# Optimization experiments

Hardware: AMD Instinct MI355X
Metric: run time of the kernel (lower is better)

The kernel has to match this reference:

```python
import jax, jax.numpy as jnp
import numpy as np

S1, S2, S3 = 1024, 1024, 32
R = 16  # r1 = r2 = r3


def setup_inputs() -> dict:
    key = jax.random.key(0)
    ks = jax.random.split(key, 7)
    # TR factors (xavier-normal-ish scale)
    Z1 = jax.random.normal(ks[0], (R, S1, R), dtype=jnp.float32) * 0.05
    Z2 = jax.random.normal(ks[1], (R, S2, R), dtype=jnp.float32) * 0.05
    Z3 = jax.random.normal(ks[2], (R, S3, R), dtype=jnp.float32) * 0.05
    # NoFC_3 conv head params (OIHW)
    W1 = jax.random.normal(ks[3], (S3, S3, 3, 3), dtype=jnp.float32) * 0.05
    b1 = jax.random.normal(ks[4], (S3,), dtype=jnp.float32) * 0.05
    W2 = jax.random.normal(ks[5], (S3, S3, 3, 3), dtype=jnp.float32) * 0.05
    b2 = jax.random.normal(ks[6], (S3,), dtype=jnp.float32) * 0.05
    return {"Z1": Z1, "Z2": Z2, "Z3": Z3, "W1": W1, "b1": b1, "W2": W2, "b2": b2}


def _leaky(x):
    # nn.LeakyReLU default negative_slope = 0.01
    return jnp.where(x >= 0, x, 0.01 * x)


def _conv(x, W, b):
    # 3x3, stride 1, SAME padding, NCHW / OIHW
    y = jax.lax.conv_general_dilated(
        x, W, window_strides=(1, 1), padding="SAME",
        dimension_numbers=("NCHW", "OIHW", "NCHW"))
    return y + b[None, :, None, None]


def reference(Z1, Z2, Z3, W1, b1, W2, b2):
    # tr_product: X[i,j,k] = sum_{a,b,c} Z1[a,i,b] Z2[b,j,c] Z3[c,k,a]
    # Contract small factors first to avoid an O(S1*S2) rank-expanded intermediate.
    T = jnp.einsum("cka,aib->kicb", Z3, Z1)        # (S3, S1, r3, r2) — small
    X = jnp.einsum("kicb,bjc->ijk", T, Z2)         # (S1, S2, S3)
    # NoHiT.forward: permute(2,1,0).unsqueeze(0) -> (1, S3, S2, S1)
    x = X.transpose(2, 1, 0)[None]
    x = _leaky(_conv(x, W1, b1))
    x = _leaky(_conv(x, W2, b2))
    # squeeze(0).permute(1,2,0) -> (S2, S1, S3)
    return x[0].transpose(1, 2, 0)
```

## Files before the change

### kernel.cpp

```cpp
#include <hip/hip_runtime.h>

typedef short  s16x4 __attribute__((ext_vector_type(4)));
typedef short  s16x8 __attribute__((ext_vector_type(8)));
typedef float  f32x4 __attribute__((ext_vector_type(4)));
typedef float  f32x16 __attribute__((ext_vector_type(16)));

__device__ __forceinline__ unsigned short f2b(float f) {
    unsigned u = __float_as_uint(f);
    u = u + 0x7FFFu + ((u >> 16) & 1u);
    return (unsigned short)(u >> 16);
}

__device__ __forceinline__ void gload16(const void* g, void* l) {
    __builtin_amdgcn_global_load_lds((const __attribute__((address_space(1))) unsigned*)g,
                                     (__attribute__((address_space(3))) unsigned*)l,
                                     16, 0, 0);
}

__device__ __forceinline__ int swz(int x) { return (x ^ (x >> 2)) & 3; }
__device__ __forceinline__ int f2s(int o) { return (o >> 1) & 3; }

__global__ __launch_bounds__(256) void v_kernel(const float* __restrict__ Z2,
                                                const float* __restrict__ Z3,
                                                short* __restrict__ Bv2) {
    __shared__ float z3t[8192];
    __shared__ float z2s[256];
    const int tid = threadIdx.x, j = blockIdx.x;
    for (int t = tid; t < 8192; t += 256) {
        float v = Z3[t];
        int c = t >> 9, k = (t >> 4) & 31, a = t & 15;
        z3t[c * 512 + a * 32 + k] = v;
    }
    z2s[tid] = Z2[(tid >> 4) * 16384 + j * 16 + (tid & 15)];
    __syncthreads();
    const int a = tid >> 4, b = tid & 15;
    float z2r[16];
    #pragma unroll
    for (int c = 0; c < 16; ++c) z2r[c] = z2s[b * 16 + c];
    float s[32];
    #pragma unroll
    for (int k = 0; k < 32; ++k) s[k] = 0.f;
    #pragma unroll
    for (int c = 0; c < 16; ++c) {
        #pragma unroll
        for (int k4 = 0; k4 < 8; ++k4) {
            f32x4 v = *(const f32x4*)&z3t[c * 512 + a * 32 + k4 * 4];
            #pragma unroll
            for (int r = 0; r < 4; ++r) s[k4 * 4 + r] += z2r[c] * v[r];
        }
    }
    #pragma unroll
    for (int k = 0; k < 32; ++k)
        Bv2[(size_t)(j * 32 + k) * 256 + tid] = (short)f2b(s[k]);
}

__global__ __launch_bounds__(256) void z1r_kernel(const float* __restrict__ Z1,
                                                  short* __restrict__ Z1r) {
    __shared__ float z1s[4096];
    const int tid = threadIdx.x, i0 = blockIdx.x * 16;
    #pragma unroll
    for (int a = 0; a < 16; ++a)
        z1s[a * 256 + tid] = Z1[a * 16384 + i0 * 16 + tid];
    __syncthreads();
    #pragma unroll
    for (int il = 0; il < 16; ++il)
        Z1r[(size_t)(i0 + il) * 256 + tid] =
            (short)f2b(z1s[(tid >> 4) * 256 + il * 16 + (tid & 15)]);
}

__global__ __launch_bounds__(256) void gemm_kernel(const short* __restrict__ Bv2,
                                                   const short* __restrict__ Z1r,
                                                   short* __restrict__ X) {
    __shared__ short sA[128 * 32];
    __shared__ short sB[128 * 32];
    const int tid = threadIdx.x;
    const int w = tid >> 6, lane = tid & 63, lane15 = lane & 15, q = lane >> 4;
    const int wm = w >> 1, wn = w & 1;
    const int bid = blockIdx.x;
    const int l = (bid & 7) * 256 + (bid >> 3);
    const int n0 = (l >> 3) * 128, i0 = (l & 7) * 128;
    const int rs = lane >> 2, sp = lane & 3;
    const int scol = (sp ^ swz(rs)) << 3;
    const int fl = swz(lane15);

    f32x4 acc[4][4];
    #pragma unroll
    for (int a = 0; a < 4; ++a)
        #pragma unroll
        for (int b = 0; b < 4; ++b) acc[a][b] = (f32x4)0;

    for (int kk = 0; kk < 256; kk += 32) {
        gload16(&Bv2[(size_t)(n0 + w * 16 + rs) * 256 + kk + scol],       (char*)sA + w * 1024);
        gload16(&Bv2[(size_t)(n0 + (w + 4) * 16 + rs) * 256 + kk + scol], (char*)sA + (w + 4) * 1024);
        gload16(&Z1r[(size_t)(i0 + w * 16 + rs) * 256 + kk + scol],       (char*)sB + w * 1024);
        gload16(&Z1r[(size_t)(i0 + (w + 4) * 16 + rs) * 256 + kk + scol], (char*)sB + (w + 4) * 1024);
        __syncthreads();
        s16x8 af[4], bf[4];
        #pragma unroll
        for (int fm = 0; fm < 4; ++fm) {
            const int r = wm * 64 + fm * 16 + lane15;
            af[fm] = *(const s16x8*)&sA[r * 32 + ((q ^ fl) << 3)];
        }
        #pragma unroll
        for (int fn = 0; fn < 4; ++fn) {
            const int r = wn * 64 + fn * 16 + lane15;
            bf[fn] = *(const s16x8*)&sB[r * 32 + ((q ^ fl) << 3)];
        }
        #pragma unroll
        for (int fm = 0; fm < 4; ++fm)
            #pragma unroll
            for (int fn = 0; fn < 4; ++fn)
                acc[fm][fn] = __builtin_amdgcn_mfma_f32_16x16x32_bf16(af[fm], bf[fn], acc[fm][fn], 0, 0, 0);
        __syncthreads();
    }

    #pragma unroll
    for (int fm = 0; fm < 4; ++fm) {
        const int nbase = n0 + wm * 64 + fm * 16;
        const int j = nbase >> 5;
        const int k0 = (nbase & 31) + q * 4;
        #pragma unroll
        for (int fn = 0; fn < 4; ++fn) {
            const int i = i0 + wn * 64 + fn * 16 + lane15;
            s16x4 p;
            #pragma unroll
            for (int r = 0; r < 4; ++r) p[r] = (short)f2b(acc[fm][fn][r]);
            *(s16x4*)&X[(size_t)j * 32768 + i * 32 + k0] = p;
        }
    }
}

#define XWN 130
#define XRN (XWN * 32)
__global__ __launch_bounds__(512) void fconv_kernel(const short* __restrict__ in,
                                                    const float* __restrict__ W1,
                                                    const float* __restrict__ b1,
                                                    const float* __restrict__ W2,
                                                    const float* __restrict__ b2,
                                                    float* __restrict__ out) {
    __shared__ short xr[4 * XRN];
    __shared__ short yr[4 * XRN];
    const int tid = threadIdx.x;
    const int w = tid >> 6, lane = tid & 63, r31 = lane & 31, h = lane >> 5;
    const int bx = blockIdx.x, by = blockIdx.y;
    const int x0 = bx * 126, y0 = by * 16;
    const bool isC1 = (w < 4);
    const int tb = isC1 ? (w * 32 - 1) : ((w - 4) * 32);

    s16x8 aw[9][2];
    {
        const float* Ws = isC1 ? W1 : W2;
        #pragma unroll
        for (int t = 0; t < 9; ++t)
            #pragma unroll
            for (int kh = 0; kh < 2; ++kh) {
                const int c0 = kh * 16 + h * 8;
                s16x8 a;
                #pragma unroll
                for (int e = 0; e < 8; ++e)
                    a[e] = (short)f2b(Ws[(r31 * 32 + c0 + e) * 9 + t]);
                aw[t][kh] = a;
            }
    }
    f32x4 bb[4];
    {
        const float* bs = isC1 ? b1 : b2;
        #pragma unroll
        for (int g = 0; g < 4; ++g) bb[g] = *(const f32x4*)&bs[g * 8 + h * 4];
    }

    if (bx == 0 || bx == 8) {
        s16x8* p = (s16x8*)xr;
        for (int i = tid; i < 4 * XWN * 4; i += 512) p[i] = (s16x8)0;
        __syncthreads();
    }

    auto stage = [&](int rho) {
        const int gy = y0 + rho;
        char* base = (char*)&xr[((rho + 4) & 3) * XRN];
        if ((unsigned)gy < 1024u) {
            {
                const int ox = tid >> 2, u = tid & 3;
                const int gx = x0 - 2 + ox;
                if ((unsigned)gx < 1024u)
                    gload16(&in[(size_t)((gy << 10) + gx) * 32 + ((u ^ f2s(ox)) << 3)],
                            base + (w * 64) * 16);
            }
            {
                const int idx = 512 + tid;
                if (idx < XWN * 4) {
                    const int ox = idx >> 2, u = idx & 3;
                    const int gx = x0 - 2 + ox;
                    if ((unsigned)gx < 1024u)
                        gload16(&in[(size_t)((gy << 10) + gx) * 32 + ((u ^ f2s(ox)) << 3)],
                                base + 512 * 16);
                }
            }
        } else {
            s16x8* b8 = (s16x8*)base;
            for (int i = tid; i < XWN * 4; i += 512) b8[i] = (s16x8)0;
        }
    };

    auto conv1_row = [&](int ry) {
        const int gy1 = y0 + ry;
        const int ysl = ((ry + 4) & 3) * XRN;
        if ((unsigned)gy1 < 1024u) {
            int xs[3];
            #pragma unroll
            for (int dy = 0; dy < 3; ++dy) xs[dy] = ((ry - 1 + dy + 4) & 3) * XRN;
            f32x16 acc = (f32x16)0;
            #pragma unroll
            for (int dy = 0; dy < 3; ++dy)
                #pragma unroll
                for (int dx = 0; dx < 3; ++dx) {
                    const int ox = tb + r31 + dx + 1;
                    const int fo = f2s(ox);
                    #pragma unroll
                    for (int kh = 0; kh < 2; ++kh) {
                        const s16x8 bfr = *(const s16x8*)&xr[xs[dy] + ox * 32 + (((kh * 2 + h) ^ fo) << 3)];
                        acc = __builtin_amdgcn_mfma_f32_32x32x16_bf16(aw[dy * 3 + dx][kh], bfr, acc, 0, 0, 0);
                    }
                }
            const int p = tb + r31;
            const int oy = p + 1;
            const int gx1 = x0 + p;
            const bool valid = (unsigned)gx1 < 1024u;
            const int fo = f2s(oy);
            #pragma unroll
            for (int g = 0; g < 4; ++g) {
                s16x4 pk;
                #pragma unroll
                for (int e = 0; e < 4; ++e) {
                    float f = acc[g * 4 + e] + bb[g][e];
                    f = f >= 0.f ? f : 0.01f * f;
                    pk[e] = valid ? (short)f2b(f) : (short)0;
                }
                *(s16x4*)&yr[ysl + oy * 32 + ((g ^ fo) << 3) + h * 4] = pk;
            }
        } else {
            s16x8* b8 = (s16x8*)&yr[ysl];
            for (int i = tid; i < XWN * 4; i += 256) b8[i] = (s16x8)0;
        }
    };

    auto conv2_row = [&](int ro) {
        const int gy = y0 + ro;
        int ys[3];
        #pragma unroll
        for (int dy = 0; dy < 3; ++dy) ys[dy] = ((ro - 1 + dy + 4) & 3) * XRN;
        f32x16 acc = (f32x16)0;
        #pragma unroll
        for (int dy = 0; dy < 3; ++dy)
            #pragma unroll
            for (int dx = 0; dx < 3; ++dx) {
                const int oy = tb + r31 + dx;
                const int fo = f2s(oy);
                #pragma unroll
                for (int kh = 0; kh < 2; ++kh) {
                    const s16x8 bfr = *(const s16x8*)&yr[ys[dy] + oy * 32 + (((kh * 2 + h) ^ fo) << 3)];
                    acc = __builtin_amdgcn_mfma_f32_32x32x16_bf16(aw[dy * 3 + dx][kh], bfr, acc, 0, 0, 0);
                }
            }
        const int px = tb + r31;
        const int gx = x0 + px;
        if (px < 126 && gx < 1024) {
            #pragma unroll
            for (int g = 0; g < 4; ++g) {
                f32x4 v;
                #pragma unroll
                for (int e = 0; e < 4; ++e) {
                    float f = acc[g * 4 + e] + bb[g][e];
                    v[e] = f >= 0.f ? f : 0.01f * f;
                }
                *(f32x4*)&out[(size_t)((gy << 10) + gx) * 32 + g * 8 + h * 4] = v;
            }
        }
    };

    stage(-2); stage(-1); stage(0);
    __syncthreads();

    for (int t = 0; t <= 18; ++t) {
        if (t <= 16) stage(t + 1);
        if (isC1) { if (t <= 17) conv1_row(t - 1); }
        else      { if (t >= 3)  conv2_row(t - 3); }
        __syncthreads();
    }
}

extern "C" void kernel_launch(void* const* d_in, const int* in_sizes, int n_in,
                              void* d_out, int out_size, void* d_ws, size_t ws_size,
                              hipStream_t stream) {
    const float* Z1 = (const float*)d_in[0];
    const float* Z2 = (const float*)d_in[1];
    const float* Z3 = (const float*)d_in[2];
    const float* W1 = (const float*)d_in[3];
    const float* b1 = (const float*)d_in[4];
    const float* W2 = (const float*)d_in[5];
    const float* b2 = (const float*)d_in[6];

    short* X   = (short*)d_ws;
    short* Bv2 = (short*)d_out;
    short* Z1r = Bv2 + 8388608;

    v_kernel  <<<1024, 256, 0, stream>>>(Z2, Z3, Bv2);
    z1r_kernel<<<64,   256, 0, stream>>>(Z1, Z1r);
    gemm_kernel<<<2048, 256, 0, stream>>>(Bv2, Z1r, X);
    fconv_kernel<<<dim3(9, 64), 512, 0, stream>>>(X, W1, b1, W2, b2, (float*)d_out);
}
```

Measured before the change: 151.4 us.

## Make fused conv per-wave independent with direct global loads and no block barriers

The two-conv kernel is restructured so each wave owns its own 30-column by 16-row strip and does conv1 then conv2 itself. Conv1 now loads its input straight from global memory into registers instead of staging rows through shared memory. Intermediate rows go into a small per-wave LDS ring, so the kernel needs no block-wide __syncthreads and no split between producer and consumer waves. In exchange, each wave computes 32 columns to produce 30, and overlapping input rows and columns are re-read from global memory through the caches.

Result: slower. 240.8 us (+59.0%).

```diff
diff --git a/kernel.cpp b/kernel.cpp
--- a/kernel.cpp
+++ b/kernel.cpp
@@ -130,162 +130,141 @@
     }
 }
 
-#define XWN 130
-#define XRN (XWN * 32)
-__global__ __launch_bounds__(512) void fconv_kernel(const short* __restrict__ in,
+#define YRS (34 * 32)
+__global__ __launch_bounds__(256) void fconv_kernel(const short* __restrict__ in,
                                                     const float* __restrict__ W1,
                                                     const float* __restrict__ b1,
                                                     const float* __restrict__ W2,
                                                     const float* __restrict__ b2,
                                                     float* __restrict__ out) {
-    __shared__ short xr[4 * XRN];
-    __shared__ short yr[4 * XRN];
+    __shared__ short yb[4 * 3 * YRS];
     const int tid = threadIdx.x;
-    const int w = tid >> 6, lane = tid & 63, r31 = lane & 31, h = lane >> 5;
-    const int bx = blockIdx.x, by = blockIdx.y;
-    const int x0 = bx * 126, y0 = by * 16;
-    const bool isC1 = (w < 4);
-    const int tb = isC1 ? (w * 32 - 1) : ((w - 4) * 32);
-
-    s16x8 aw[9][2];
+    const int w = tid >> 6, lane = tid & 63, p = lane & 31, h = lane >> 5;
+    const int job = blockIdx.x * 4 + w;
+    const int st = job % 35, bnd = job / 35;
+    const int sx0 = st * 30, y0 = bnd * 16;
+    short* ybw = &yb[w * 3 * YRS];
+
+    s16x8 aw1[9][2], aw2[9][2];
     {
-        const float* Ws = isC1 ? W1 : W2;
         #pragma unroll
         for (int t = 0; t < 9; ++t)
             #pragma unroll
             for (int kh = 0; kh < 2; ++kh) {
                 const int c0 = kh * 16 + h * 8;
-                s16x8 a;
-                #pragma unroll
-                for (int e = 0; e < 8; ++e)
-                    a[e] = (short)f2b(Ws[(r31 * 32 + c0 + e) * 9 + t]);
-                aw[t][kh] = a;
-            }
-    }
-    f32x4 bb[4];
-    {
-        const float* bs = isC1 ? b1 : b2;
-        #pragma unroll
-        for (int g = 0; g < 4; ++g) bb[g] = *(const f32x4*)&bs[g * 8 + h * 4];
-    }
-
-    if (bx == 0 || bx == 8) {
-        s16x8* p = (s16x8*)xr;
-        for (int i = tid; i < 4 * XWN * 4; i += 512) p[i] = (s16x8)0;
-        __syncthreads();
-    }
-
-    auto stage = [&](int rho) {
-        const int gy = y0 + rho;
-        char* base = (char*)&xr[((rho + 4) & 3) * XRN];
-        if ((unsigned)gy < 1024u) {
-            {
-                const int ox = tid >> 2, u = tid & 3;
-                const int gx = x0 - 2 + ox;
-                if ((unsigned)gx < 1024u)
-                    gload16(&in[(size_t)((gy << 10) + gx) * 32 + ((u ^ f2s(ox)) << 3)],
-                            base + (w * 64) * 16);
-            }
-            {
-                const int idx = 512 + tid;
-                if (idx < XWN * 4) {
-                    const int ox = idx >> 2, u = idx & 3;
-                    const int gx = x0 - 2 + ox;
-                    if ((unsigned)gx < 1024u)
-                        gload16(&in[(size_t)((gy << 10) + gx) * 32 + ((u ^ f2s(ox)) << 3)],
-                                base + 512 * 16);
-                }
-            }
-        } else {
-            s16x8* b8 = (s16x8*)base;
-            for (int i = tid; i < XWN * 4; i += 512) b8[i] = (s16x8)0;
-        }
-    };
-
-    auto conv1_row = [&](int ry) {
-        const int gy1 = y0 + ry;
-        const int ysl = ((ry + 4) & 3) * XRN;
-        if ((unsigned)gy1 < 1024u) {
-            int xs[3];
-            #pragma unroll
-            for (int dy = 0; dy < 3; ++dy) xs[dy] = ((ry - 1 + dy + 4) & 3) * XRN;
+                s16x8 a1, a2;
+                #pragma unroll
+                for (int e = 0; e < 8; ++e) {
+                    a1[e] = (short)f2b(W1[(p * 32 + c0 + e) * 9 + t]);
+                    a2[e] = (short)f2b(W2[(p * 32 + c0 + e) * 9 + t]);
+                }
+                aw1[t][kh] = a1; aw2[t][kh] = a2;
+            }
+    }
+    f32x4 bb1[4], bb2[4];
+    #pragma unroll
+    for (int g = 0; g < 4; ++g) {
+        bb1[g] = *(const f32x4*)&b1[g * 8 + h * 4];
+        bb2[g] = *(const f32x4*)&b2[g * 8 + h * 4];
+    }
+
+    bool pxok[3];
+    #pragma unroll
+    for (int dx = 0; dx < 3; ++dx) pxok[dx] = (unsigned)(sx0 - 2 + p + dx) < 1024u;
+    const bool y1ok = (unsigned)(sx0 - 1 + p) < 1024u;
+    const int gx = sx0 + p;
+    const bool outok = (p < 30) && (gx < 1024);
+    const int fop = f2s(p);
+
+    for (int rr = 0; rr <= 18; ++rr) {
+        const int ry = y0 - 1 + rr;
+
+        s16x8 xf2[6];
+        {
+            const int gy = ry + 1;
+            const bool rok = (rr <= 17) && ((unsigned)gy < 1024u);
+            const short* rbase = in + (((size_t)gy << 10) + (sx0 - 2 + p)) * 32 + h * 8;
+            #pragma unroll
+            for (int dx = 0; dx < 3; ++dx)
+                #pragma unroll
+                for (int kh = 0; kh < 2; ++kh) {
+                    s16x8 v = (s16x8)0;
+                    if (rok && pxok[dx]) v = *(const s16x8*)(rbase + dx * 32 + kh * 16);
+                    xf2[dx * 2 + kh] = v;
+                }
+        }
+
+        if (rr >= 3) {
+            const int ro = y0 + rr - 3;
             f32x16 acc = (f32x16)0;
             #pragma unroll
-            for (int dy = 0; dy < 3; ++dy)
+            for (int dy = 0; dy < 3; ++dy) {
+                const int ysl = ((rr - 3 + dy) % 3) * YRS;
                 #pragma unroll
                 for (int dx = 0; dx < 3; ++dx) {
-                    const int ox = tb + r31 + dx + 1;
-                    const int fo = f2s(ox);
+                    const int idx = p + dx;
+                    const int fo = f2s(idx);
                     #pragma unroll
                     for (int kh = 0; kh < 2; ++kh) {
-                        const s16x8 bfr = *(const s16x8*)&xr[xs[dy] + ox * 32 + (((kh * 2 + h) ^ fo) << 3)];
-                        acc = __builtin_amdgcn_mfma_f32_32x32x16_bf16(aw[dy * 3 + dx][kh], bfr, acc, 0, 0, 0);
+                        const s16x8 bfr = *(const s16x8*)&ybw[ysl + idx * 32 + (((kh * 2 + h) ^ fo) << 3)];
+                        acc = __builtin_amdgcn_mfma_f32_32x32x16_bf16(aw2[dy * 3 + dx][kh], bfr, acc, 0, 0, 0);
                     }
                 }
-            const int p = tb + r31;
-            const int oy = p + 1;
-            const int gx1 = x0 + p;
-            const bool valid = (unsigned)gx1 < 1024u;
-            const int fo = f2s(oy);
-            #pragma unroll
-            for (int g = 0; g < 4; ++g) {
-                s16x4 pk;
-                #pragma unroll
-                for (int e = 0; e < 4; ++e) {
-                    float f = acc[g * 4 + e] + bb[g][e];
-                    f = f >= 0.f ? f : 0.01f * f;
-                    pk[e] = valid ? (short)f2b(f) : (short)0;
-                }
-                *(s16x4*)&yr[ysl + oy * 32 + ((g ^ fo) << 3) + h * 4] = pk;
-            }
-        } else {
-            s16x8* b8 = (s16x8*)&yr[ysl];
-            for (int i = tid; i < XWN * 4; i += 256) b8[i] = (s16x8)0;
-        }
-    };
-
-    auto conv2_row = [&](int ro) {
-        const int gy = y0 + ro;
-        int ys[3];
-        #pragma unroll
-        for (int dy = 0; dy < 3; ++dy) ys[dy] = ((ro - 1 + dy + 4) & 3) * XRN;
-        f32x16 acc = (f32x16)0;
-        #pragma unroll
-        for (int dy = 0; dy < 3; ++dy)
-            #pragma unroll
-            for (int dx = 0; dx < 3; ++dx) {
-                const int oy = tb + r31 + dx;
-                const int fo = f2s(oy);
-                #pragma unroll
-                for (int kh = 0; kh < 2; ++kh) {
-                    const s16x8 bfr = *(const s16x8*)&yr[ys[dy] + oy * 32 + (((kh * 2 + h) ^ fo) << 3)];
-                    acc = __builtin_amdgcn_mfma_f32_32x32x16_bf16(aw[dy * 3 + dx][kh], bfr, acc, 0, 0, 0);
-                }
-            }
-        const int px = tb + r31;
-        const int gx = x0 + px;
-        if (px < 126 && gx < 1024) {
-            #pragma unroll
-            for (int g = 0; g < 4; ++g) {
-                f32x4 v;
-                #pragma unroll
-                for (int e = 0; e < 4; ++e) {
-                    float f = acc[g * 4 + e] + bb[g][e];
-                    v[e] = f >= 0.f ? f : 0.01f * f;
-                }
-                *(f32x4*)&out[(size_t)((gy << 10) + gx) * 32 + g * 8 + h * 4] = v;
-            }
-        }
-    };
-
-    stage(-2); stage(-1); stage(0);
-    __syncthreads();
-
-    for (int t = 0; t <= 18; ++t) {
-        if (t <= 16) stage(t + 1);
-        if (isC1) { if (t <= 17) conv1_row(t - 1); }
-        else      { if (t >= 3)  conv2_row(t - 3); }
-        __syncthreads();
+            }
+            if (outok) {
+                #pragma unroll
+                for (int g = 0; g < 4; ++g) {
+                    f32x4 v;
+                    #pragma unroll
+                    for (int e = 0; e < 4; ++e) {
+                        float f = acc[g * 4 + e] + bb2[g][e];
+                        v[e] = f >= 0.f ? f : 0.01f * f;
+                    }
+                    *(f32x4*)&out[(((size_t)ro << 10) + gx) * 32 + g * 8 + h * 4] = v;
+                }
+            }
+        }
+
+        if (rr <= 17) {
+            const int ysl = (rr % 3) * YRS;
+            if ((unsigned)ry < 1024u) {
+                f32x16 acc = (f32x16)0;
+                #pragma unroll
+                for (int dy = 0; dy < 2; ++dy) {
+                    const int gy = ry - 1 + dy;
+                    const bool rok = (unsigned)gy < 1024u;
+                    const short* rbase = in + (((size_t)gy << 10) + (sx0 - 2 + p)) * 32 + h * 8;
+                    #pragma unroll
+                    for (int dx = 0; dx < 3; ++dx)
+                        #pragma unroll
+                        for (int kh = 0; kh < 2; ++kh) {
+                            s16x8 v = (s16x8)0;
+                            if (rok && pxok[dx]) v = *(const s16x8*)(rbase + dx * 32 + kh * 16);
+                            acc = __builtin_amdgcn_mfma_f32_32x32x16_bf16(aw1[dy * 3 + dx][kh], v, acc, 0, 0, 0);
+                        }
+                }
+                #pragma unroll
+                for (int dx = 0; dx < 3; ++dx)
+                    #pragma unroll
+                    for (int kh = 0; kh < 2; ++kh)
+                        acc = __builtin_amdgcn_mfma_f32_32x32x16_bf16(aw1[6 + dx][kh], xf2[dx * 2 + kh], acc, 0, 0, 0);
+                #pragma unroll
+                for (int g = 0; g < 4; ++g) {
+                    s16x4 pk;
+                    #pragma unroll
+                    for (int e = 0; e < 4; ++e) {
+                        float f = acc[g * 4 + e] + bb1[g][e];
+                        f = f >= 0.f ? f : 0.01f * f;
+                        pk[e] = y1ok ? (short)f2b(f) : (short)0;
+                    }
+                    *(s16x4*)&ybw[ysl + p * 32 + ((g ^ fop) << 3) + h * 4] = pk;
+                }
+            } else {
+                #pragma unroll
+                for (int g = 0; g < 4; ++g)
+                    *(s16x4*)&ybw[ysl + p * 32 + ((g ^ fop) << 3) + h * 4] = (s16x4)0;
+            }
+        }
     }
 }
 
@@ -307,5 +286,5 @@
     v_kernel  <<<1024, 256, 0, stream>>>(Z2, Z3, Bv2);
     z1r_kernel<<<64,   256, 0, stream>>>(Z1, Z1r);
     gemm_kernel<<<2048, 256, 0, stream>>>(Bv2, Z1r, X);
-    fconv_kernel<<<dim3(9, 64), 512, 0, stream>>>(X, W1, b1, W2, b2, (float*)d_out);
-}
+    fconv_kernel<<<560, 256, 0, stream>>>(X, W1, b1, W2, b2, (float*)d_out);
+}
```
